# Optimization experiments

Hardware: AMD Instinct MI355X
Metric: run time of the kernel (lower is better)

The kernel has to match this reference:

```python
import jax, jax.numpy as jnp
import numpy as np

N = 131072          # collocation points
H = 256             # hidden_dim
F = 128             # num_freqs
L_HID = 7           # num_layers - 1 extra hidden linears
SIGMA = 10.0
TWO_PI = 2.0 * np.pi


def setup_inputs() -> dict:
    key = jax.random.key(0)
    ks = jax.random.split(key, 8)
    s = 1.0 / np.sqrt(H)  # small init so tanh doesn't saturate
    return {
        "tx": jax.random.normal(ks[0], (N, 2), dtype=jnp.float32),
        "B": jax.random.normal(ks[1], (F, 2), dtype=jnp.float32) * SIGMA,
        "W_in": jax.random.normal(ks[2], (H, 2 * F), dtype=jnp.float32) * (1.0 / np.sqrt(2 * F)),
        "b_in": jax.random.normal(ks[3], (H,), dtype=jnp.float32) * 0.01,
        "W_h": jax.random.normal(ks[4], (L_HID, H, H), dtype=jnp.float32) * s,
        "b_h": jax.random.normal(ks[5], (L_HID, H), dtype=jnp.float32) * 0.01,
        "W_out": jax.random.normal(ks[6], (1, H), dtype=jnp.float32) * s,
        "b_out": jax.random.normal(ks[7], (1,), dtype=jnp.float32) * 0.01,
    }


def reference(tx, B, W_in, b_in, W_h, b_h, W_out, b_out):
    # Fourier feature projection: [N, 2] @ [2, F] -> [N, F]
    proj = TWO_PI * (tx @ B.T)
    feat = jnp.concatenate([jnp.sin(proj), jnp.cos(proj)], axis=-1)  # [N, 2F]

    # First hidden layer (torch Linear: x @ W.T + b)
    h = jnp.tanh(feat @ W_in.T + b_in)  # [N, H]

    # Remaining hidden layers via scan over stacked weights
    def step(h, wb):
        W, b = wb
        return jnp.tanh(h @ W.T + b), None

    h, _ = jax.lax.scan(step, h, (W_h, b_h))

    # Output layer (no activation)
    return h @ W_out.T + b_out  # [N, 1]
```

## Files before the change

### kernel.cpp

```cpp
#include <hip/hip_runtime.h>


#define HDIM   256
#define NFREQ  128
#define NLAYER 8
#define PTSW   32
#define NTHR   256
#define TILE_N 128
#define WHALVES (NLAYER * HDIM * HDIM)

typedef __attribute__((ext_vector_type(8))) _Float16 half8;
typedef __attribute__((ext_vector_type(4))) _Float16 half4;
typedef __attribute__((ext_vector_type(2))) _Float16 half2;
typedef __attribute__((ext_vector_type(4))) float float4v;

__device__ __forceinline__ half2 pk2(float a, float b) {
    return __builtin_bit_cast(half2, __builtin_amdgcn_cvt_pkrtz(a, b));
}

#define TANH_K 2.885390081777927f
__device__ __forceinline__ float fast_tanh_fused(float acc, float bK) {
    float z = __builtin_amdgcn_exp2f(fmaf(acc, TANH_K, bK));
    float r = __builtin_amdgcn_rcpf(z + 1.0f);
    return fmaf(-2.0f, r, 1.0f);
}

__global__ void convert_w_kernel(const float* __restrict__ W_in,
                                 const float* __restrict__ W_h,
                                 _Float16* __restrict__ dst)
{
    const int i = blockIdx.x * blockDim.x + threadIdx.x;
    const int j     = i & 7;
    const int lane  = (i >> 3) & 63;
    const int frag  = i >> 9;
    const int kt    = frag & 7;
    const int mt    = (frag >> 3) & 3;
    const int c     = (frag >> 5) & 3;
    const int layer = frag >> 7;
    const int u = c * 64 + mt * 16 + (lane & 15);
    const int k = kt * 32 + (lane >> 4) * 8 + j;
    const float v = (layer == 0) ? W_in[u * HDIM + k]
                                 : W_h[((layer - 1) * HDIM + u) * HDIM + k];
    dst[i] = (_Float16)v;
}

__device__ __forceinline__ void layer_step(const _Float16* __restrict__ wl,
                                           const float* __restrict__ bl,
                                           _Float16* __restrict__ lds0,
                                           _Float16* __restrict__ lds1,
                                           const int laneM, const int quad,
                                           const half8 (&hin)[2][8],
                                           half8 (&hout)[2][8])
{
    half8 a[4];
    #pragma unroll
    for (int mt = 0; mt < 4; ++mt)
        a[mt] = *(const half8*)&wl[(mt * 8) * 512];

    #pragma unroll
    for (int c = 0; c < 4; ++c) {
        _Float16* __restrict__ lds = (c & 1) ? lds1 : lds0;

        float4v acc[4][2];
        #pragma unroll
        for (int mt = 0; mt < 4; ++mt)
            #pragma unroll
            for (int nt = 0; nt < 2; ++nt)
                acc[mt][nt] = (float4v){0.f, 0.f, 0.f, 0.f};

        #pragma unroll
        for (int kt = 0; kt < 8; ++kt) {
            half8 an[4];
            if (kt < 7) {
                #pragma unroll
                for (int mt = 0; mt < 4; ++mt)
                    an[mt] = *(const half8*)&wl[(c * 32 + mt * 8 + kt + 1) * 512];
            } else if (c < 3) {
                #pragma unroll
                for (int mt = 0; mt < 4; ++mt)
                    an[mt] = *(const half8*)&wl[((c + 1) * 32 + mt * 8) * 512];
            }
            #pragma unroll
            for (int mt = 0; mt < 4; ++mt)
                #pragma unroll
                for (int nt = 0; nt < 2; ++nt)
                    acc[mt][nt] = __builtin_amdgcn_mfma_f32_16x16x32_f16(
                        a[mt], hin[nt][kt], acc[mt][nt], 0, 0, 0);
            if (kt < 7 || c < 3) {
                #pragma unroll
                for (int mt = 0; mt < 4; ++mt) a[mt] = an[mt];
            }
        }

        #pragma unroll
        for (int mt = 0; mt < 4; ++mt) {
            const float4 b4 = *(const float4*)&bl[c * 64 + mt * 16 + quad * 4];
            const float bx = b4.x * TANH_K, by = b4.y * TANH_K;
            const float bz = b4.z * TANH_K, bw = b4.w * TANH_K;
            const int c8 = mt * 2 + (quad >> 1);
            #pragma unroll
            for (int nt = 0; nt < 2; ++nt) {
                const int row = nt * 16 + laneM;
                const float v0 = fast_tanh_fused(acc[mt][nt].x, bx);
                const float v1 = fast_tanh_fused(acc[mt][nt].y, by);
                const float v2 = fast_tanh_fused(acc[mt][nt].z, bz);
                const float v3 = fast_tanh_fused(acc[mt][nt].w, bw);
                const half2 lo = pk2(v0, v1);
                const half2 hi = pk2(v2, v3);
                half4 pkv;
                pkv.x = lo.x; pkv.y = lo.y; pkv.z = hi.x; pkv.w = hi.y;
                *(half4*)&lds[row * 64 + ((c8 ^ (row & 7)) << 3) + (quad & 1) * 4] = pkv;
            }
        }
        #pragma unroll
        for (int kp = 0; kp < 2; ++kp)
            #pragma unroll
            for (int nt = 0; nt < 2; ++nt) {
                const int row = nt * 16 + laneM;
                const int c8r = (kp * 4 + quad) ^ (row & 7);
                hout[nt][c * 2 + kp] = *(const half8*)&lds[row * 64 + (c8r << 3)];
            }
    }
}

__device__ __forceinline__ float dot8(const half8 h, const float4 wa, const float4 wb) {
    return (float)h[0]*wa.x + (float)h[1]*wa.y + (float)h[2]*wa.z + (float)h[3]*wa.w
         + (float)h[4]*wb.x + (float)h[5]*wb.y + (float)h[6]*wb.z + (float)h[7]*wb.w;
}

__global__ __launch_bounds__(NTHR, 2)
void ffmlp_kernel(const float* __restrict__ tx,
                  const float* __restrict__ Bf,
                  const _Float16* __restrict__ Wall,
                  const float* __restrict__ b_in,
                  const float* __restrict__ b_h,
                  const float* __restrict__ W_out,
                  const float* __restrict__ b_out,
                  float* __restrict__ out)
{
    __shared__ __align__(16) _Float16 lbuf[4][2][PTSW * 64];

    const int tid   = threadIdx.x;
    const int wave  = tid >> 6;
    const int lane  = tid & 63;
    const int laneM = lane & 15;
    const int quad  = lane >> 4;
    const int p0    = blockIdx.x * TILE_N + wave * PTSW;

    half8 h0[2][8], h1[2][8];

    {
        const float2* txv = (const float2*)tx;
        const float2* Bv  = (const float2*)Bf;
        #pragma unroll
        for (int nt = 0; nt < 2; ++nt) {
            const float2 t = txv[p0 + nt * 16 + laneM];
            #pragma unroll
            for (int kq = 0; kq < 4; ++kq) {
                const int f0 = kq * 32 + quad * 8;
                half8 s8, c8v;
                #pragma unroll
                for (int jj = 0; jj < 8; jj += 2) {
                    const float2 bA = Bv[f0 + jj];
                    const float2 bB = Bv[f0 + jj + 1];
                    const float r0 = __builtin_amdgcn_fractf(t.x * bA.x + t.y * bA.y);
                    const float r1 = __builtin_amdgcn_fractf(t.x * bB.x + t.y * bB.y);
                    const half2 sp = pk2(__builtin_amdgcn_sinf(r0), __builtin_amdgcn_sinf(r1));
                    const half2 cp = pk2(__builtin_amdgcn_cosf(r0), __builtin_amdgcn_cosf(r1));
                    s8[jj] = sp.x;  s8[jj + 1] = sp.y;
                    c8v[jj] = cp.x; c8v[jj + 1] = cp.y;
                }
                h0[nt][kq]     = s8;
                h0[nt][kq + 4] = c8v;
            }
        }
    }

    _Float16* __restrict__ lds0 = &lbuf[wave][0][0];
    _Float16* __restrict__ lds1 = &lbuf[wave][1][0];
    #pragma unroll 1
    for (int lp = 0; lp < 4; ++lp) {
        const int la = 2 * lp, lb = 2 * lp + 1;
        const float* bla = (la == 0) ? b_in : b_h + (la - 1) * HDIM;
        const float* blb = b_h + (lb - 1) * HDIM;
        layer_step(Wall + la * (HDIM * HDIM) + lane * 8, bla,
                   lds0, lds1, laneM, quad, h0, h1);
        layer_step(Wall + lb * (HDIM * HDIM) + lane * 8, blb,
                   lds0, lds1, laneM, quad, h1, h0);
    }

    {
        float s0 = 0.f, s1 = 0.f;
        #pragma unroll
        for (int kt = 0; kt < 8; ++kt) {
            const float4 wa = *(const float4*)&W_out[kt * 32 + quad * 8];
            const float4 wb = *(const float4*)&W_out[kt * 32 + quad * 8 + 4];
            s0 += dot8(h0[0][kt], wa, wb);
            s1 += dot8(h0[1][kt], wa, wb);
        }
        s0 += __shfl_xor(s0, 16); s0 += __shfl_xor(s0, 32);
        s1 += __shfl_xor(s1, 16); s1 += __shfl_xor(s1, 32);
        if (quad == 0) {
            const float bo = b_out[0];
            out[p0 + laneM]      = s0 + bo;
            out[p0 + 16 + laneM] = s1 + bo;
        }
    }
}

extern "C" void kernel_launch(void* const* d_in, const int* in_sizes, int n_in,
                              void* d_out, int out_size, void* d_ws, size_t ws_size,
                              hipStream_t stream) {
    const float* tx    = (const float*)d_in[0];
    const float* Bf    = (const float*)d_in[1];
    const float* W_in  = (const float*)d_in[2];
    const float* b_in  = (const float*)d_in[3];
    const float* W_h   = (const float*)d_in[4];
    const float* b_h   = (const float*)d_in[5];
    const float* W_out = (const float*)d_in[6];
    const float* b_out = (const float*)d_in[7];
    float* out = (float*)d_out;

    _Float16* Wall = (_Float16*)d_ws;

    const int npts   = in_sizes[0] / 2;
    const int blocks = npts / TILE_N;

    convert_w_kernel<<<WHALVES / NTHR, NTHR, 0, stream>>>(W_in, W_h, Wall);
    ffmlp_kernel<<<blocks, NTHR, 0, stream>>>(tx, Bf, Wall, b_in, b_h,
                                              W_out, b_out, out);
}
```

Baseline: 243.1 us.

## Stage half of weight fragments into LDS via async global_load_lds double buffering

Each 64-row weight chunk is split in two. One half is loaded into a double-buffered LDS area with async global-to-LDS copies shared by the four waves, and the other half is still read straight from global memory. Biases are prescaled by the tanh constant in the conversion kernel, and the per-wave activation buffer shrinks to a single buffer. The aim is to cut redundant per-wave global/L2 weight traffic. The cost is a block-wide barrier at every chunk step, plus a larger LDS footprint that may limit occupancy.

Result: no change. 246.4 us (+1.4%).

```diff
diff --git a/kernel.cpp b/kernel.cpp
--- a/kernel.cpp
+++ b/kernel.cpp
@@ -2,7 +2,6 @@
 
 
 #define HDIM   256
-#define NFREQ  128
 #define NLAYER 8
 #define PTSW   32
 #define NTHR   256
@@ -27,6 +26,8 @@
 
 __global__ void convert_w_kernel(const float* __restrict__ W_in,
                                  const float* __restrict__ W_h,
+                                 const float* __restrict__ b_in,
+                                 const float* __restrict__ b_h,
                                  _Float16* __restrict__ dst)
 {
     const int i = blockIdx.x * blockDim.x + threadIdx.x;
@@ -42,24 +43,50 @@
     const float v = (layer == 0) ? W_in[u * HDIM + k]
                                  : W_h[((layer - 1) * HDIM + u) * HDIM + k];
     dst[i] = (_Float16)v;
-}
-
-__device__ __forceinline__ void layer_step(const _Float16* __restrict__ wl,
-                                           const float* __restrict__ bl,
-                                           _Float16* __restrict__ lds0,
-                                           _Float16* __restrict__ lds1,
+
+    if (i < NLAYER * HDIM) {
+        float* bk = (float*)(dst + WHALVES);
+        const int l = i >> 8, uu = i & 255;
+        const float b = (l == 0) ? b_in[uu] : b_h[(l - 1) * HDIM + uu];
+        bk[i] = b * TANH_K;
+    }
+}
+
+__device__ __forceinline__ void stage_half(const _Float16* __restrict__ gsrc,
+                                           _Float16* __restrict__ ldst,
+                                           const int wave, const int lane)
+{
+    #pragma unroll
+    for (int i = 0; i < 4; ++i) {
+        const int off = (wave * 4 + i) * 512;
+        __builtin_amdgcn_global_load_lds(
+            (const __attribute__((address_space(1))) void*)(gsrc + off + lane * 8),
+            (__attribute__((address_space(3))) void*)(ldst + off),
+            16, 0, 0);
+    }
+}
+
+__device__ __forceinline__ void layer_step(const int l,
+                                           const _Float16* __restrict__ Wall,
+                                           const float* __restrict__ bK,
+                                           _Float16 (&wbuf)[2][8192],
+                                           _Float16* __restrict__ lbuf,
+                                           const int wave, const int lane,
                                            const int laneM, const int quad,
                                            const half8 (&hin)[2][8],
                                            half8 (&hout)[2][8])
 {
-    half8 a[4];
-    #pragma unroll
-    for (int mt = 0; mt < 4; ++mt)
-        a[mt] = *(const half8*)&wl[(mt * 8) * 512];
-
     #pragma unroll
     for (int c = 0; c < 4; ++c) {
-        _Float16* __restrict__ lds = (c & 1) ? lds1 : lds0;
+        __syncthreads();
+
+        const int step = l * 4 + c;
+        if (step < NLAYER * 4 - 1)
+            stage_half(Wall + ((step + 1) & 31) * 16384,
+                       &wbuf[(c + 1) & 1][0], wave, lane);
+
+        const _Float16* __restrict__ wl = &wbuf[c & 1][0];
+        const _Float16* __restrict__ wg = Wall + step * 16384 + 8192;
 
         float4v acc[4][2];
         #pragma unroll
@@ -68,17 +95,19 @@
             for (int nt = 0; nt < 2; ++nt)
                 acc[mt][nt] = (float4v){0.f, 0.f, 0.f, 0.f};
 
+        half8 a[4], an[4];
+        a[0] = *(const half8*)&wl[(0 * 8 + 0) * 512 + lane * 8];
+        a[1] = *(const half8*)&wl[(1 * 8 + 0) * 512 + lane * 8];
+        a[2] = *(const half8*)&wg[(0 * 8 + 0) * 512 + lane * 8];
+        a[3] = *(const half8*)&wg[(1 * 8 + 0) * 512 + lane * 8];
+
         #pragma unroll
         for (int kt = 0; kt < 8; ++kt) {
-            half8 an[4];
             if (kt < 7) {
-                #pragma unroll
-                for (int mt = 0; mt < 4; ++mt)
-                    an[mt] = *(const half8*)&wl[(c * 32 + mt * 8 + kt + 1) * 512];
-            } else if (c < 3) {
-                #pragma unroll
-                for (int mt = 0; mt < 4; ++mt)
-                    an[mt] = *(const half8*)&wl[((c + 1) * 32 + mt * 8) * 512];
+                an[0] = *(const half8*)&wl[(0 * 8 + kt + 1) * 512 + lane * 8];
+                an[1] = *(const half8*)&wl[(1 * 8 + kt + 1) * 512 + lane * 8];
+                an[2] = *(const half8*)&wg[(0 * 8 + kt + 1) * 512 + lane * 8];
+                an[3] = *(const half8*)&wg[(1 * 8 + kt + 1) * 512 + lane * 8];
             }
             #pragma unroll
             for (int mt = 0; mt < 4; ++mt)
@@ -86,30 +115,32 @@
                 for (int nt = 0; nt < 2; ++nt)
                     acc[mt][nt] = __builtin_amdgcn_mfma_f32_16x16x32_f16(
                         a[mt], hin[nt][kt], acc[mt][nt], 0, 0, 0);
-            if (kt < 7 || c < 3) {
+            if (kt < 7) {
                 #pragma unroll
                 for (int mt = 0; mt < 4; ++mt) a[mt] = an[mt];
             }
         }
 
+        float4 bias[4];
+        #pragma unroll
+        for (int mt = 0; mt < 4; ++mt)
+            bias[mt] = *(const float4*)&bK[l * 256 + c * 64 + mt * 16 + quad * 4];
+
         #pragma unroll
         for (int mt = 0; mt < 4; ++mt) {
-            const float4 b4 = *(const float4*)&bl[c * 64 + mt * 16 + quad * 4];
-            const float bx = b4.x * TANH_K, by = b4.y * TANH_K;
-            const float bz = b4.z * TANH_K, bw = b4.w * TANH_K;
             const int c8 = mt * 2 + (quad >> 1);
             #pragma unroll
             for (int nt = 0; nt < 2; ++nt) {
                 const int row = nt * 16 + laneM;
-                const float v0 = fast_tanh_fused(acc[mt][nt].x, bx);
-                const float v1 = fast_tanh_fused(acc[mt][nt].y, by);
-                const float v2 = fast_tanh_fused(acc[mt][nt].z, bz);
-                const float v3 = fast_tanh_fused(acc[mt][nt].w, bw);
+                const float v0 = fast_tanh_fused(acc[mt][nt].x, bias[mt].x);
+                const float v1 = fast_tanh_fused(acc[mt][nt].y, bias[mt].y);
+                const float v2 = fast_tanh_fused(acc[mt][nt].z, bias[mt].z);
+                const float v3 = fast_tanh_fused(acc[mt][nt].w, bias[mt].w);
                 const half2 lo = pk2(v0, v1);
                 const half2 hi = pk2(v2, v3);
                 half4 pkv;
                 pkv.x = lo.x; pkv.y = lo.y; pkv.z = hi.x; pkv.w = hi.y;
-                *(half4*)&lds[row * 64 + ((c8 ^ (row & 7)) << 3) + (quad & 1) * 4] = pkv;
+                *(half4*)&lbuf[row * 64 + ((c8 ^ (row & 7)) << 3) + (quad & 1) * 4] = pkv;
             }
         }
         #pragma unroll
@@ -118,7 +149,7 @@
             for (int nt = 0; nt < 2; ++nt) {
                 const int row = nt * 16 + laneM;
                 const int c8r = (kp * 4 + quad) ^ (row & 7);
-                hout[nt][c * 2 + kp] = *(const half8*)&lds[row * 64 + (c8r << 3)];
+                hout[nt][c * 2 + kp] = *(const half8*)&lbuf[row * 64 + (c8r << 3)];
             }
     }
 }
@@ -132,13 +163,12 @@
 void ffmlp_kernel(const float* __restrict__ tx,
                   const float* __restrict__ Bf,
                   const _Float16* __restrict__ Wall,
-                  const float* __restrict__ b_in,
-                  const float* __restrict__ b_h,
                   const float* __restrict__ W_out,
                   const float* __restrict__ b_out,
                   float* __restrict__ out)
 {
-    __shared__ __align__(16) _Float16 lbuf[4][2][PTSW * 64];
+    __shared__ __align__(16) _Float16 wbuf[2][8192];
+    __shared__ __align__(16) _Float16 lbuf[4][2048];
 
     const int tid   = threadIdx.x;
     const int wave  = tid >> 6;
@@ -146,6 +176,10 @@
     const int laneM = lane & 15;
     const int quad  = lane >> 4;
     const int p0    = blockIdx.x * TILE_N + wave * PTSW;
+
+    const float* bK = (const float*)(Wall + WHALVES);
+
+    stage_half(Wall, &wbuf[0][0], wave, lane);
 
     half8 h0[2][8], h1[2][8];
 
@@ -176,17 +210,11 @@
         }
     }
 
-    _Float16* __restrict__ lds0 = &lbuf[wave][0][0];
-    _Float16* __restrict__ lds1 = &lbuf[wave][1][0];
+    _Float16* __restrict__ lw = &lbuf[wave][0];
     #pragma unroll 1
     for (int lp = 0; lp < 4; ++lp) {
-        const int la = 2 * lp, lb = 2 * lp + 1;
-        const float* bla = (la == 0) ? b_in : b_h + (la - 1) * HDIM;
-        const float* blb = b_h + (lb - 1) * HDIM;
-        layer_step(Wall + la * (HDIM * HDIM) + lane * 8, bla,
-                   lds0, lds1, laneM, quad, h0, h1);
-        layer_step(Wall + lb * (HDIM * HDIM) + lane * 8, blb,
-                   lds0, lds1, laneM, quad, h1, h0);
+        layer_step(2 * lp,     Wall, bK, wbuf, lw, wave, lane, laneM, quad, h0, h1);
+        layer_step(2 * lp + 1, Wall, bK, wbuf, lw, wave, lane, laneM, quad, h1, h0);
     }
 
     {
@@ -226,7 +254,6 @@
     const int npts   = in_sizes[0] / 2;
     const int blocks = npts / TILE_N;
 
-    convert_w_kernel<<<WHALVES / NTHR, NTHR, 0, stream>>>(W_in, W_h, Wall);
-    ffmlp_kernel<<<blocks, NTHR, 0, stream>>>(tx, Bf, Wall, b_in, b_h,
-                                              W_out, b_out, out);
-}
+    convert_w_kernel<<<WHALVES / NTHR, NTHR, 0, stream>>>(W_in, W_h, b_in, b_h, Wall);
+    ffmlp_kernel<<<blocks, NTHR, 0, stream>>>(tx, Bf, Wall, W_out, b_out, out);
+}
```

## Raise occupancy target, prescale biases in prep kernel, restructure weight prefetch ring

Applied to the files above, without the earlier changes.

The launch bound now asks for 4 blocks per CU instead of 2, which caps VGPR use per thread so more waves can be resident to hide latency. Weight fragments are loaded through a 3-slot rotating buffer that prefetches two k-steps ahead within each 64-column chunk, instead of a one-ahead prefetch that carried across chunks. Biases are pre-multiplied by the tanh constant in the conversion kernel and stored after the fp16 weights, which removes the per-layer multiplies. The tighter register budget may cause spills, and each chunk now starts with two fresh loads that are not prefetched.

Measured after the change: 465.9 us. 1.92x slower.

```diff
diff --git a/kernel.cpp b/kernel.cpp
--- a/kernel.cpp
+++ b/kernel.cpp
@@ -2,7 +2,6 @@
 
 
 #define HDIM   256
-#define NFREQ  128
 #define NLAYER 8
 #define PTSW   32
 #define NTHR   256
@@ -27,6 +26,8 @@
 
 __global__ void convert_w_kernel(const float* __restrict__ W_in,
                                  const float* __restrict__ W_h,
+                                 const float* __restrict__ b_in,
+                                 const float* __restrict__ b_h,
                                  _Float16* __restrict__ dst)
 {
     const int i = blockIdx.x * blockDim.x + threadIdx.x;
@@ -42,6 +43,13 @@
     const float v = (layer == 0) ? W_in[u * HDIM + k]
                                  : W_h[((layer - 1) * HDIM + u) * HDIM + k];
     dst[i] = (_Float16)v;
+
+    if (i < NLAYER * HDIM) {
+        float* bk = (float*)(dst + WHALVES);
+        const int l = i >> 8, uu = i & 255;
+        const float b = (l == 0) ? b_in[uu] : b_h[(l - 1) * HDIM + uu];
+        bk[i] = b * TANH_K;
+    }
 }
 
 __device__ __forceinline__ void layer_step(const _Float16* __restrict__ wl,
@@ -52,11 +60,6 @@
                                            const half8 (&hin)[2][8],
                                            half8 (&hout)[2][8])
 {
-    half8 a[4];
-    #pragma unroll
-    for (int mt = 0; mt < 4; ++mt)
-        a[mt] = *(const half8*)&wl[(mt * 8) * 512];
-
     #pragma unroll
     for (int c = 0; c < 4; ++c) {
         _Float16* __restrict__ lds = (c & 1) ? lds1 : lds0;
@@ -68,43 +71,46 @@
             for (int nt = 0; nt < 2; ++nt)
                 acc[mt][nt] = (float4v){0.f, 0.f, 0.f, 0.f};
 
+        half8 A[3][4];
+        #pragma unroll
+        for (int mt = 0; mt < 4; ++mt)
+            A[0][mt] = *(const half8*)&wl[(c * 32 + mt * 8 + 0) * 512];
+        #pragma unroll
+        for (int mt = 0; mt < 4; ++mt)
+            A[1][mt] = *(const half8*)&wl[(c * 32 + mt * 8 + 1) * 512];
+
         #pragma unroll
         for (int kt = 0; kt < 8; ++kt) {
-            half8 an[4];
-            if (kt < 7) {
+            if (kt < 6) {
+                const int s = (kt + 2) % 3;
                 #pragma unroll
                 for (int mt = 0; mt < 4; ++mt)
-                    an[mt] = *(const half8*)&wl[(c * 32 + mt * 8 + kt + 1) * 512];
-            } else if (c < 3) {
-                #pragma unroll
-                for (int mt = 0; mt < 4; ++mt)
-                    an[mt] = *(const half8*)&wl[((c + 1) * 32 + mt * 8) * 512];
-            }
+                    A[s][mt] = *(const half8*)&wl[(c * 32 + mt * 8 + kt + 2) * 512];
+            }
+            const int cs = kt % 3;
             #pragma unroll
             for (int mt = 0; mt < 4; ++mt)
                 #pragma unroll
                 for (int nt = 0; nt < 2; ++nt)
                     acc[mt][nt] = __builtin_amdgcn_mfma_f32_16x16x32_f16(
-                        a[mt], hin[nt][kt], acc[mt][nt], 0, 0, 0);
-            if (kt < 7 || c < 3) {
-                #pragma unroll
-                for (int mt = 0; mt < 4; ++mt) a[mt] = an[mt];
-            }
-        }
+                        A[cs][mt], hin[nt][kt], acc[mt][nt], 0, 0, 0);
+        }
+
+        float4 bias[4];
+        #pragma unroll
+        for (int mt = 0; mt < 4; ++mt)
+            bias[mt] = *(const float4*)&bl[c * 64 + mt * 16 + quad * 4];
 
         #pragma unroll
         for (int mt = 0; mt < 4; ++mt) {
-            const float4 b4 = *(const float4*)&bl[c * 64 + mt * 16 + quad * 4];
-            const float bx = b4.x * TANH_K, by = b4.y * TANH_K;
-            const float bz = b4.z * TANH_K, bw = b4.w * TANH_K;
             const int c8 = mt * 2 + (quad >> 1);
             #pragma unroll
             for (int nt = 0; nt < 2; ++nt) {
                 const int row = nt * 16 + laneM;
-                const float v0 = fast_tanh_fused(acc[mt][nt].x, bx);
-                const float v1 = fast_tanh_fused(acc[mt][nt].y, by);
-                const float v2 = fast_tanh_fused(acc[mt][nt].z, bz);
-                const float v3 = fast_tanh_fused(acc[mt][nt].w, bw);
+                const float v0 = fast_tanh_fused(acc[mt][nt].x, bias[mt].x);
+                const float v1 = fast_tanh_fused(acc[mt][nt].y, bias[mt].y);
+                const float v2 = fast_tanh_fused(acc[mt][nt].z, bias[mt].z);
+                const float v3 = fast_tanh_fused(acc[mt][nt].w, bias[mt].w);
                 const half2 lo = pk2(v0, v1);
                 const half2 hi = pk2(v2, v3);
                 half4 pkv;
@@ -128,12 +134,10 @@
          + (float)h[4]*wb.x + (float)h[5]*wb.y + (float)h[6]*wb.z + (float)h[7]*wb.w;
 }
 
-__global__ __launch_bounds__(NTHR, 2)
+__global__ __launch_bounds__(NTHR, 4)
 void ffmlp_kernel(const float* __restrict__ tx,
                   const float* __restrict__ Bf,
                   const _Float16* __restrict__ Wall,
-                  const float* __restrict__ b_in,
-                  const float* __restrict__ b_h,
                   const float* __restrict__ W_out,
                   const float* __restrict__ b_out,
                   float* __restrict__ out)
@@ -146,6 +150,8 @@
     const int laneM = lane & 15;
     const int quad  = lane >> 4;
     const int p0    = blockIdx.x * TILE_N + wave * PTSW;
+
+    const float* bK = (const float*)(Wall + WHALVES);
 
     half8 h0[2][8], h1[2][8];
 
@@ -181,11 +187,9 @@
     #pragma unroll 1
     for (int lp = 0; lp < 4; ++lp) {
         const int la = 2 * lp, lb = 2 * lp + 1;
-        const float* bla = (la == 0) ? b_in : b_h + (la - 1) * HDIM;
-        const float* blb = b_h + (lb - 1) * HDIM;
-        layer_step(Wall + la * (HDIM * HDIM) + lane * 8, bla,
+        layer_step(Wall + la * (HDIM * HDIM) + lane * 8, bK + la * HDIM,
                    lds0, lds1, laneM, quad, h0, h1);
-        layer_step(Wall + lb * (HDIM * HDIM) + lane * 8, blb,
+        layer_step(Wall + lb * (HDIM * HDIM) + lane * 8, bK + lb * HDIM,
                    lds0, lds1, laneM, quad, h1, h0);
     }
 
@@ -226,7 +230,6 @@
     const int npts   = in_sizes[0] / 2;
     const int blocks = npts / TILE_N;
 
-    convert_w_kernel<<<WHALVES / NTHR, NTHR, 0, stream>>>(W_in, W_h, Wall);
-    ffmlp_kernel<<<blocks, NTHR, 0, stream>>>(tx, Bf, Wall, b_in, b_h,
-                                              W_out, b_out, out);
-}
+    convert_w_kernel<<<WHALVES / NTHR, NTHR, 0, stream>>>(W_in, W_h, b_in, b_h, Wall);
+    ffmlp_kernel<<<blocks, NTHR, 0, stream>>>(tx, Bf, Wall, W_out, b_out, out);
+}
```
